# Kernel tuning notes

Measured on AMD Instinct MI355X. Metric: run time of the kernel, lower is better.

## Reference

```python
import jax, jax.numpy as jnp
import numpy as np

MAX_NEIGHBORS = 10
D = 1024
N = 16384

def setup_inputs() -> dict:
    key = jax.random.key(0)
    ks = jax.random.split(key, 12)
    s = 0.05
    inp = {
        'target_embedding': jax.random.normal(ks[0], (D,), jnp.float32),
        'all_embeddings': jax.random.normal(ks[1], (N, D), jnp.float32),
        'similarity_matrix': jax.random.normal(ks[2], (N, N), jnp.float32),
        # attention_net: Linear(2D->D), ReLU, Linear(D->1)
        'W_att1': jax.random.normal(ks[3], (2 * D, D), jnp.float32) * s,
        'b_att1': jnp.zeros((D,), jnp.float32),
        'W_att2': jax.random.normal(ks[4], (D, 1), jnp.float32) * s,
        'b_att2': jnp.zeros((1,), jnp.float32),
        # neighbor_count_net: Linear(D->D//2), ReLU, Linear(D//2->1), Sigmoid
        'W_cnt1': jax.random.normal(ks[5], (D, D // 2), jnp.float32) * s,
        'b_cnt1': jnp.zeros((D // 2,), jnp.float32),
        'W_cnt2': jax.random.normal(ks[6], (D // 2, 1), jnp.float32) * s,
        'b_cnt2': jnp.zeros((1,), jnp.float32),
        'target_idx': 123,
    }
    return inp

def reference(target_embedding, all_embeddings, similarity_matrix,
              W_att1, b_att1, W_att2, b_att2,
              W_cnt1, b_cnt1, W_cnt2, b_cnt2, target_idx):
    # dynamic neighbor count: int(sigmoid(mlp(x)) * max_neighbors), clamped to [1, max_neighbors]
    h = jax.nn.relu(target_embedding @ W_cnt1 + b_cnt1)
    frac = jax.nn.sigmoid(h @ W_cnt2 + b_cnt2)[0]
    dynamic_k = jnp.clip(jnp.floor(frac * MAX_NEIGHBORS).astype(jnp.int32), 1, MAX_NEIGHBORS)

    # top-(K+1) over the target's similarity row; statically sized, mask to dynamic_k
    row = similarity_matrix[target_idx]
    _, top_idx = jax.lax.top_k(row, MAX_NEIGHBORS + 1)  # [K+1]
    # stable compaction: move target_idx (if present) to the end, keep order otherwise
    order = jnp.where(top_idx == target_idx, MAX_NEIGHBORS + 1, jnp.arange(MAX_NEIGHBORS + 1))
    neighbor_idx = top_idx[jnp.argsort(order)][:MAX_NEIGHBORS]  # [K]
    valid = jnp.arange(MAX_NEIGHBORS) < dynamic_k              # [K]

    neighbor_emb = all_embeddings[neighbor_idx]                 # [K, D]
    target_exp = jnp.broadcast_to(target_embedding, (MAX_NEIGHBORS, D))
    pair = jnp.concatenate([target_exp, neighbor_emb], axis=-1)  # [K, 2D]
    scores = (jax.nn.relu(pair @ W_att1 + b_att1) @ W_att2 + b_att2)[:, 0]  # [K]
    scores = jnp.where(valid, scores, -jnp.inf)
    weights = jax.nn.softmax(scores)                            # zeros at invalid slots
    aggregated = weights @ neighbor_emb                         # [D]
    return aggregated, weights, neighbor_idx, weights
```

## Files before the change

kernel.cpp:

```cpp
#include <hip/hip_runtime.h>
#include <math.h>

#define NN 16384
#define DD 1024
#define HD 512

#define WS_DK  0
#define WS_NB  4
#define WS_SC  16
#define WS_UP  64
#define WS_HP  (64 + 32 * 1024)

__global__ void __launch_bounds__(512) k1(const float* __restrict__ x,
                                          const float* __restrict__ W1,
                                          const float* __restrict__ Wc1,
                                          const float* __restrict__ sim,
                                          const int* __restrict__ tidx,
                                          float* __restrict__ ws,
                                          float* __restrict__ out) {
    const int t = threadIdx.x;
    const int b = blockIdx.x;
    const int lane = t & 63, wave = t >> 6;

    if (b > 0 && b <= 64) {
        __shared__ float xs[32];
        const int idx = b - 1, ic = idx >> 1, jc = idx & 1;
        const int ibase = ic * 32;
        if (t < 32) xs[t] = x[ibase + t];
        __syncthreads();
        const int j = jc * 512 + t;
        float acc = 0.f;
        const float* W = W1 + (size_t)ibase * DD + j;
        #pragma unroll 8
        for (int ii = 0; ii < 32; ++ii) acc += xs[ii] * W[(size_t)ii * DD];
        ws[WS_UP + ic * DD + j] = acc;
        return;
    }
    if (b > 64) {
        __shared__ float xs[32];
        const int c = b - 65;
        const int ibase = c * 32;
        if (t < 32) xs[t] = x[ibase + t];
        __syncthreads();
        float acc = 0.f;
        const float* W = Wc1 + (size_t)ibase * HD + t;
        #pragma unroll 8
        for (int ii = 0; ii < 32; ++ii) acc += xs[ii] * W[(size_t)ii * HD];
        ws[WS_HP + c * HD + t] = acc;
        return;
    }

    if (t < 10) ws[WS_SC + t] = 0.f;

    const int tgt = tidx[0];
    const float4* row4 = (const float4*)(sim + (size_t)tgt * NN);
    float vals[32];
    #pragma unroll
    for (int c = 0; c < 8; ++c) {
        float4 v = row4[c * 512 + t];
        vals[c * 4 + 0] = v.x; vals[c * 4 + 1] = v.y;
        vals[c * 4 + 2] = v.z; vals[c * 4 + 3] = v.w;
    }
    unsigned used = 0u;
    float bv = -INFINITY; int bs = 0;
    #pragma unroll
    for (int s = 0; s < 32; ++s) if (vals[s] > bv) { bv = vals[s]; bs = s; }

    __shared__ float wlv[8][11];
    __shared__ int   wli[8][11];

    for (int it = 0; it < 11; ++it) {
        float cv = bv;
        int   cg = (bs >> 2) * 2048 + t * 4 + (bs & 3);
        #pragma unroll
        for (int off = 32; off > 0; off >>= 1) {
            float ov = __shfl_down(cv, off);
            int   og = __shfl_down(cg, off);
            if (ov > cv || (ov == cv && og < cg)) { cv = ov; cg = og; }
        }
        const int wg = __shfl(cg, 0);
        if (lane == 0) { wlv[wave][it] = cv; wli[wave][it] = cg; }
        if (((wg >> 2) & 511) == t) {
            used |= 1u << (((wg >> 11) << 2) | (wg & 3));
            bv = -INFINITY; bs = 0;
            #pragma unroll
            for (int s = 0; s < 32; ++s) {
                float v = ((used >> s) & 1u) ? -INFINITY : vals[s];
                if (v > bv) { bv = v; bs = s; }
            }
        }
    }
    __syncthreads();
    if (t == 0) {
        int head[8] = {0, 0, 0, 0, 0, 0, 0, 0};
        int toplist[11];
        for (int it = 0; it < 11; ++it) {
            float fv = -INFINITY; int fg = 0x7fffffff; int fw = 0;
            #pragma unroll
            for (int w = 0; w < 8; ++w) {
                float v = wlv[w][head[w]];
                int   g = wli[w][head[w]];
                if (v > fv || (v == fv && g < fg)) { fv = v; fg = g; fw = w; }
            }
            toplist[it] = fg;
            head[fw] = head[fw] < 10 ? head[fw] + 1 : 10;
        }
        int cnt = 0;
        int* nbp = (int*)ws + WS_NB;
        for (int i = 0; i < 11 && cnt < 10; ++i) {
            int v = toplist[i];
            if (v != tgt) { nbp[cnt] = v; out[1034 + cnt] = (float)v; ++cnt; }
        }
    }
}

__global__ void __launch_bounds__(512) k2(const float* __restrict__ emb,
                                          const float* __restrict__ W1,
                                          const float* __restrict__ ba1,
                                          const float* __restrict__ W2,
                                          const float* __restrict__ bc1,
                                          const float* __restrict__ Wc2,
                                          const float* __restrict__ bc2,
                                          float* __restrict__ ws) {
    const int t = threadIdx.x;
    const int b = blockIdx.x;
    const int lane = t & 63, wave = t >> 6;

    __shared__ int    nb[10];
    __shared__ float4 es4[10][256];
    __shared__ float  red[32][16][11];
    __shared__ float  ured[32][17];
    __shared__ float  scr[16][10];
    __shared__ float  redp[8];

    if (b == 64) {
        float s = 0.f;
        #pragma unroll 8
        for (int c = 0; c < 32; ++c) s += ws[WS_HP + c * HD + t];
        float v = fmaxf(s + bc1[t], 0.f) * Wc2[t];
        #pragma unroll
        for (int off = 32; off > 0; off >>= 1) v += __shfl_down(v, off);
        if (lane == 0) redp[wave] = v;
        __syncthreads();
        if (t == 0) {
            float z = bc2[0];
            #pragma unroll
            for (int w = 0; w < 8; ++w) z += redp[w];
            float frac = 1.f / (1.f + expf(-z));
            int dk = (int)floorf(frac * 10.f);
            ((int*)ws)[WS_DK] = dk < 1 ? 1 : (dk > 10 ? 10 : dk);
        }
        return;
    }

    const int jl  = t & 15;
    const int seg = t >> 4;
    const int jg  = b * 16 + jl;

    if (t < 10) nb[t] = ((const int*)ws)[WS_NB + t];
    __syncthreads();
    #pragma unroll
    for (int i = t; i < 2560; i += 512) {
        int k = i >> 8, c = i & 255;
        es4[k][c] = ((const float4*)(emb + (size_t)nb[k] * DD))[c];
    }
    ured[seg][jl] = ws[WS_UP + seg * DD + jg];
    __syncthreads();

    float acc[10];
    #pragma unroll
    for (int k = 0; k < 10; ++k) acc[k] = 0.f;
    const float* Wb = W1 + (size_t)(1024 + seg * 32) * DD + jg;
    for (int c = 0; c < 8; ++c) {
        float4 ev[10];
        #pragma unroll
        for (int k = 0; k < 10; ++k) ev[k] = es4[k][seg * 8 + c];
        #pragma unroll
        for (int q = 0; q < 4; ++q) {
            const float wb = Wb[(size_t)(c * 4 + q) * DD];
            #pragma unroll
            for (int k = 0; k < 10; ++k)
                acc[k] += reinterpret_cast<const float*>(&ev[k])[q] * wb;
        }
    }
    #pragma unroll
    for (int k = 0; k < 10; ++k) red[seg][jl][k] = acc[k];
    __syncthreads();

    if (t < 160) {
        const int k = t >> 4, jj = t & 15;
        float s = 0.f;
        #pragma unroll 8
        for (int g = 0; g < 32; ++g) s += red[g][jj][k];
        float u = 0.f;
        #pragma unroll 8
        for (int g = 0; g < 32; ++g) u += ured[g][jj];
        scr[jj][k] = fmaxf(u + s + ba1[b * 16 + jj], 0.f) * W2[b * 16 + jj];
    }
    __syncthreads();
    if (t < 10) {
        float s = 0.f;
        #pragma unroll
        for (int c = 0; c < 16; ++c) s += scr[c][t];
        atomicAdd(&ws[WS_SC + t], s);
    }
}

__global__ void __launch_bounds__(1024) k3(const float* __restrict__ emb,
                                           const float* __restrict__ ba2,
                                           float* __restrict__ ws,
                                           float* __restrict__ out) {
    const int t = threadIdx.x;
    __shared__ float wl[10];
    __shared__ int   nb[10];
    if (t < 10) nb[t] = ((const int*)ws)[WS_NB + t];
    if (t == 0) {
        const int dk = ((const int*)ws)[WS_DK];
        float sv[10];
        float m = -INFINITY;
        for (int k = 0; k < 10; ++k) {
            float s = ws[WS_SC + k] + ba2[0];
            sv[k] = (k < dk) ? s : -INFINITY;
            if (sv[k] > m) m = sv[k];
        }
        float sum = 0.f;
        for (int k = 0; k < 10; ++k) { sv[k] = expf(sv[k] - m); sum += sv[k]; }
        for (int k = 0; k < 10; ++k) wl[k] = sv[k] / sum;
    }
    __syncthreads();
    float a = 0.f;
    #pragma unroll
    for (int k = 0; k < 10; ++k) a += wl[k] * emb[(size_t)nb[k] * DD + t];
    out[t] = a;
    if (t < 10) { out[1024 + t] = wl[t]; out[1044 + t] = wl[t]; }
}

extern "C" void kernel_launch(void* const* d_in, const int* in_sizes, int n_in,
                              void* d_out, int out_size, void* d_ws, size_t ws_size,
                              hipStream_t stream) {
    const float* x    = (const float*)d_in[0];
    const float* emb  = (const float*)d_in[1];
    const float* sim  = (const float*)d_in[2];
    const float* W1   = (const float*)d_in[3];
    const float* ba1  = (const float*)d_in[4];
    const float* W2   = (const float*)d_in[5];
    const float* ba2  = (const float*)d_in[6];
    const float* Wc1  = (const float*)d_in[7];
    const float* bc1  = (const float*)d_in[8];
    const float* Wc2  = (const float*)d_in[9];
    const float* bc2  = (const float*)d_in[10];
    const int*   tidx = (const int*)d_in[11];
    float* out = (float*)d_out;
    float* ws  = (float*)d_ws;

    hipLaunchKernelGGL(k1, dim3(97), dim3(512),  0, stream, x, W1, Wc1, sim, tidx, ws, out);
    hipLaunchKernelGGL(k2, dim3(65), dim3(512),  0, stream, emb, W1, ba1, W2, bc1, Wc2, bc2, ws);
    hipLaunchKernelGGL(k3, dim3(1),  dim3(1024), 0, stream, emb, ba2, ws, out);
}
```

Baseline: 38.42 us.

## Fuse top-k, attention GEMV and count MLP into one kernel, drop a launch

Merges the three-kernel pipeline into two. Each of the 64 attention blocks now recomputes the top-k over the similarity row and the target half of the first attention layer itself. This removes the separate partial-sum pass and the atomics on scores, which now go to per-block partial slots. The count MLP runs in 32 extra blocks that each produce a partial logit, and the final kernel reduces both sets of partials. The cost is redundant top-k work: every block reads the 64 KB similarity row and runs the selection, in exchange for one fewer launch and its sync point.

```diff
diff --git a/kernel.cpp b/kernel.cpp
--- a/kernel.cpp
+++ b/kernel.cpp
@@ -5,16 +5,19 @@
 #define DD 1024
 #define HD 512
 
-#define WS_DK  0
 #define WS_NB  4
-#define WS_SC  16
-#define WS_UP  64
-#define WS_HP  (64 + 32 * 1024)
-
-__global__ void __launch_bounds__(512) k1(const float* __restrict__ x,
+#define WS_ZP  32
+#define WS_SCP 64
+
+__global__ void __launch_bounds__(512) ka(const float* __restrict__ x,
+                                          const float* __restrict__ emb,
+                                          const float* __restrict__ sim,
                                           const float* __restrict__ W1,
+                                          const float* __restrict__ ba1,
+                                          const float* __restrict__ W2,
                                           const float* __restrict__ Wc1,
-                                          const float* __restrict__ sim,
+                                          const float* __restrict__ bc1,
+                                          const float* __restrict__ Wc2,
                                           const int* __restrict__ tidx,
                                           float* __restrict__ ws,
                                           float* __restrict__ out) {
@@ -22,154 +25,121 @@
     const int b = blockIdx.x;
     const int lane = t & 63, wave = t >> 6;
 
-    if (b > 0 && b <= 64) {
-        __shared__ float xs[32];
-        const int idx = b - 1, ic = idx >> 1, jc = idx & 1;
-        const int ibase = ic * 32;
-        if (t < 32) xs[t] = x[ibase + t];
-        __syncthreads();
-        const int j = jc * 512 + t;
-        float acc = 0.f;
-        const float* W = W1 + (size_t)ibase * DD + j;
+    __shared__ float xsl[1024];
+
+    if (b >= 64) {
+        __shared__ float credc[32][17];
+        __shared__ float hs[16];
+        const int c = b - 64;
+        xsl[t] = x[t]; xsl[t + 512] = x[t + 512];
+        __syncthreads();
+        const int jl = t & 15, seg = t >> 4;
+        const int jg = c * 16 + jl;
+        float a = 0.f;
+        const float* Wc = Wc1 + (size_t)(seg * 32) * HD + jg;
         #pragma unroll 8
-        for (int ii = 0; ii < 32; ++ii) acc += xs[ii] * W[(size_t)ii * DD];
-        ws[WS_UP + ic * DD + j] = acc;
+        for (int ii = 0; ii < 32; ++ii) a += xsl[seg * 32 + ii] * Wc[(size_t)ii * HD];
+        credc[seg][jl] = a;
+        __syncthreads();
+        if (t < 16) {
+            float s = 0.f;
+            #pragma unroll 8
+            for (int g = 0; g < 32; ++g) s += credc[g][t];
+            hs[t] = fmaxf(s + bc1[c * 16 + t], 0.f) * Wc2[c * 16 + t];
+        }
+        __syncthreads();
+        if (t == 0) {
+            float z = 0.f;
+            #pragma unroll
+            for (int j = 0; j < 16; ++j) z += hs[j];
+            ws[WS_ZP + c] = z;
+        }
         return;
     }
-    if (b > 64) {
-        __shared__ float xs[32];
-        const int c = b - 65;
-        const int ibase = c * 32;
-        if (t < 32) xs[t] = x[ibase + t];
-        __syncthreads();
-        float acc = 0.f;
-        const float* W = Wc1 + (size_t)ibase * HD + t;
-        #pragma unroll 8
-        for (int ii = 0; ii < 32; ++ii) acc += xs[ii] * W[(size_t)ii * HD];
-        ws[WS_HP + c * HD + t] = acc;
-        return;
-    }
-
-    if (t < 10) ws[WS_SC + t] = 0.f;
-
-    const int tgt = tidx[0];
-    const float4* row4 = (const float4*)(sim + (size_t)tgt * NN);
-    float vals[32];
-    #pragma unroll
-    for (int c = 0; c < 8; ++c) {
-        float4 v = row4[c * 512 + t];
-        vals[c * 4 + 0] = v.x; vals[c * 4 + 1] = v.y;
-        vals[c * 4 + 2] = v.z; vals[c * 4 + 3] = v.w;
-    }
-    unsigned used = 0u;
-    float bv = -INFINITY; int bs = 0;
-    #pragma unroll
-    for (int s = 0; s < 32; ++s) if (vals[s] > bv) { bv = vals[s]; bs = s; }
-
-    __shared__ float wlv[8][11];
-    __shared__ int   wli[8][11];
-
-    for (int it = 0; it < 11; ++it) {
-        float cv = bv;
-        int   cg = (bs >> 2) * 2048 + t * 4 + (bs & 3);
-        #pragma unroll
-        for (int off = 32; off > 0; off >>= 1) {
-            float ov = __shfl_down(cv, off);
-            int   og = __shfl_down(cg, off);
-            if (ov > cv || (ov == cv && og < cg)) { cv = ov; cg = og; }
-        }
-        const int wg = __shfl(cg, 0);
-        if (lane == 0) { wlv[wave][it] = cv; wli[wave][it] = cg; }
-        if (((wg >> 2) & 511) == t) {
-            used |= 1u << (((wg >> 11) << 2) | (wg & 3));
-            bv = -INFINITY; bs = 0;
-            #pragma unroll
-            for (int s = 0; s < 32; ++s) {
-                float v = ((used >> s) & 1u) ? -INFINITY : vals[s];
-                if (v > bv) { bv = v; bs = s; }
-            }
-        }
-    }
-    __syncthreads();
-    if (t == 0) {
-        int head[8] = {0, 0, 0, 0, 0, 0, 0, 0};
-        int toplist[11];
-        for (int it = 0; it < 11; ++it) {
-            float fv = -INFINITY; int fg = 0x7fffffff; int fw = 0;
-            #pragma unroll
-            for (int w = 0; w < 8; ++w) {
-                float v = wlv[w][head[w]];
-                int   g = wli[w][head[w]];
-                if (v > fv || (v == fv && g < fg)) { fv = v; fg = g; fw = w; }
-            }
-            toplist[it] = fg;
-            head[fw] = head[fw] < 10 ? head[fw] + 1 : 10;
-        }
-        int cnt = 0;
-        int* nbp = (int*)ws + WS_NB;
-        for (int i = 0; i < 11 && cnt < 10; ++i) {
-            int v = toplist[i];
-            if (v != tgt) { nbp[cnt] = v; out[1034 + cnt] = (float)v; ++cnt; }
-        }
-    }
-}
-
-__global__ void __launch_bounds__(512) k2(const float* __restrict__ emb,
-                                          const float* __restrict__ W1,
-                                          const float* __restrict__ ba1,
-                                          const float* __restrict__ W2,
-                                          const float* __restrict__ bc1,
-                                          const float* __restrict__ Wc2,
-                                          const float* __restrict__ bc2,
-                                          float* __restrict__ ws) {
-    const int t = threadIdx.x;
-    const int b = blockIdx.x;
-    const int lane = t & 63, wave = t >> 6;
-
-    __shared__ int    nb[10];
+
+    __shared__ float  wlv[8][11];
+    __shared__ int    wli[8][11];
+    __shared__ int    nbsh[10];
     __shared__ float4 es4[10][256];
     __shared__ float  red[32][16][11];
-    __shared__ float  ured[32][17];
     __shared__ float  scr[16][10];
-    __shared__ float  redp[8];
-
-    if (b == 64) {
-        float s = 0.f;
-        #pragma unroll 8
-        for (int c = 0; c < 32; ++c) s += ws[WS_HP + c * HD + t];
-        float v = fmaxf(s + bc1[t], 0.f) * Wc2[t];
-        #pragma unroll
-        for (int off = 32; off > 0; off >>= 1) v += __shfl_down(v, off);
-        if (lane == 0) redp[wave] = v;
+
+    const int tgt = tidx[0];
+    {
+        const float4* row4 = (const float4*)(sim + (size_t)tgt * NN);
+        float vals[32];
+        #pragma unroll
+        for (int c = 0; c < 8; ++c) {
+            float4 v = row4[c * 512 + t];
+            vals[c*4+0] = v.x; vals[c*4+1] = v.y; vals[c*4+2] = v.z; vals[c*4+3] = v.w;
+        }
+        unsigned used = 0u;
+        float bv = -INFINITY; int bs = 0;
+        #pragma unroll
+        for (int s = 0; s < 32; ++s) if (vals[s] > bv) { bv = vals[s]; bs = s; }
+
+        for (int it = 0; it < 11; ++it) {
+            float cv = bv;
+            int   cg2 = (bs >> 2) * 2048 + t * 4 + (bs & 3);
+            #pragma unroll
+            for (int off = 32; off > 0; off >>= 1) {
+                float ov = __shfl_down(cv, off);
+                int   og = __shfl_down(cg2, off);
+                if (ov > cv || (ov == cv && og < cg2)) { cv = ov; cg2 = og; }
+            }
+            const int wg = __shfl(cg2, 0);
+            if (lane == 0) { wlv[wave][it] = cv; wli[wave][it] = cg2; }
+            if (((wg >> 2) & 511) == t) {
+                used |= 1u << (((wg >> 11) << 2) | (wg & 3));
+                bv = -INFINITY; bs = 0;
+                #pragma unroll
+                for (int s = 0; s < 32; ++s) {
+                    float v = ((used >> s) & 1u) ? -INFINITY : vals[s];
+                    if (v > bv) { bv = v; bs = s; }
+                }
+            }
+        }
         __syncthreads();
         if (t == 0) {
-            float z = bc2[0];
-            #pragma unroll
-            for (int w = 0; w < 8; ++w) z += redp[w];
-            float frac = 1.f / (1.f + expf(-z));
-            int dk = (int)floorf(frac * 10.f);
-            ((int*)ws)[WS_DK] = dk < 1 ? 1 : (dk > 10 ? 10 : dk);
-        }
-        return;
-    }
-
-    const int jl  = t & 15;
-    const int seg = t >> 4;
-    const int jg  = b * 16 + jl;
-
-    if (t < 10) nb[t] = ((const int*)ws)[WS_NB + t];
+            int head[8] = {0,0,0,0,0,0,0,0};
+            int toplist[11];
+            for (int it = 0; it < 11; ++it) {
+                float fv = -INFINITY; int fg = 0x7fffffff; int fw = 0;
+                #pragma unroll
+                for (int w = 0; w < 8; ++w) {
+                    float v = wlv[w][head[w]];
+                    int   g = wli[w][head[w]];
+                    if (v > fv || (v == fv && g < fg)) { fv = v; fg = g; fw = w; }
+                }
+                toplist[it] = fg;
+                head[fw] = head[fw] < 10 ? head[fw] + 1 : 10;
+            }
+            int cnt = 0;
+            for (int i = 0; i < 11 && cnt < 10; ++i) {
+                int v = toplist[i];
+                if (v != tgt) {
+                    nbsh[cnt] = v;
+                    if (b == 0) { ((int*)ws)[WS_NB + cnt] = v; out[1034 + cnt] = (float)v; }
+                    ++cnt;
+                }
+            }
+        }
+    }
+    xsl[t] = x[t]; xsl[t + 512] = x[t + 512];
     __syncthreads();
     #pragma unroll
     for (int i = t; i < 2560; i += 512) {
         int k = i >> 8, c = i & 255;
-        es4[k][c] = ((const float4*)(emb + (size_t)nb[k] * DD))[c];
-    }
-    ured[seg][jl] = ws[WS_UP + seg * DD + jg];
-    __syncthreads();
-
-    float acc[10];
-    #pragma unroll
-    for (int k = 0; k < 10; ++k) acc[k] = 0.f;
+        es4[k][c] = ((const float4*)(emb + (size_t)nbsh[k] * DD))[c];
+    }
+    __syncthreads();
+
+    const int jl = t & 15, seg = t >> 4;
+    const int jg = b * 16 + jl;
+    float acc[11];
+    #pragma unroll
+    for (int k = 0; k < 11; ++k) acc[k] = 0.f;
+    const float* Wt = W1 + (size_t)(seg * 32) * DD + jg;
     const float* Wb = W1 + (size_t)(1024 + seg * 32) * DD + jg;
     for (int c = 0; c < 8; ++c) {
         float4 ev[10];
@@ -177,24 +147,24 @@
         for (int k = 0; k < 10; ++k) ev[k] = es4[k][seg * 8 + c];
         #pragma unroll
         for (int q = 0; q < 4; ++q) {
-            const float wb = Wb[(size_t)(c * 4 + q) * DD];
+            const int row = c * 4 + q;
+            const float wt = Wt[(size_t)row * DD];
+            const float wb = Wb[(size_t)row * DD];
+            acc[10] += xsl[seg * 32 + row] * wt;
             #pragma unroll
             for (int k = 0; k < 10; ++k)
                 acc[k] += reinterpret_cast<const float*>(&ev[k])[q] * wb;
         }
     }
     #pragma unroll
-    for (int k = 0; k < 10; ++k) red[seg][jl][k] = acc[k];
+    for (int k = 0; k < 11; ++k) red[seg][jl][k] = acc[k];
     __syncthreads();
 
     if (t < 160) {
         const int k = t >> 4, jj = t & 15;
-        float s = 0.f;
+        float s = 0.f, u = 0.f;
         #pragma unroll 8
-        for (int g = 0; g < 32; ++g) s += red[g][jj][k];
-        float u = 0.f;
-        #pragma unroll 8
-        for (int g = 0; g < 32; ++g) u += ured[g][jj];
+        for (int g = 0; g < 32; ++g) { s += red[g][jj][k]; u += red[g][jj][10]; }
         scr[jj][k] = fmaxf(u + s + ba1[b * 16 + jj], 0.f) * W2[b * 16 + jj];
     }
     __syncthreads();
@@ -202,24 +172,39 @@
         float s = 0.f;
         #pragma unroll
         for (int c = 0; c < 16; ++c) s += scr[c][t];
-        atomicAdd(&ws[WS_SC + t], s);
+        ws[WS_SCP + b * 10 + t] = s;
     }
 }
 
-__global__ void __launch_bounds__(1024) k3(const float* __restrict__ emb,
+__global__ void __launch_bounds__(1024) kb(const float* __restrict__ emb,
                                            const float* __restrict__ ba2,
+                                           const float* __restrict__ bc2,
                                            float* __restrict__ ws,
                                            float* __restrict__ out) {
     const int t = threadIdx.x;
+    __shared__ float sred[10][65];
+    __shared__ float zps[32];
     __shared__ float wl[10];
     __shared__ int   nb[10];
     if (t < 10) nb[t] = ((const int*)ws)[WS_NB + t];
+    if (t < 32) zps[t] = ws[WS_ZP + t];
+    if (t < 640) { const int k = t >> 6, g = t & 63; sred[k][g] = ws[WS_SCP + g * 10 + k]; }
+    __syncthreads();
+    for (int off = 32; off > 0; off >>= 1) {
+        if (t < 640) { const int k = t >> 6, g = t & 63; if (g < off) sred[k][g] += sred[k][g + off]; }
+        __syncthreads();
+    }
     if (t == 0) {
-        const int dk = ((const int*)ws)[WS_DK];
+        float z = bc2[0];
+        #pragma unroll
+        for (int c = 0; c < 32; ++c) z += zps[c];
+        const float frac = 1.f / (1.f + expf(-z));
+        int dk = (int)floorf(frac * 10.f);
+        dk = dk < 1 ? 1 : (dk > 10 ? 10 : dk);
         float sv[10];
         float m = -INFINITY;
         for (int k = 0; k < 10; ++k) {
-            float s = ws[WS_SC + k] + ba2[0];
+            float s = sred[k][0] + ba2[0];
             sv[k] = (k < dk) ? s : -INFINITY;
             if (sv[k] > m) m = sv[k];
         }
@@ -253,7 +238,7 @@
     float* out = (float*)d_out;
     float* ws  = (float*)d_ws;
 
-    hipLaunchKernelGGL(k1, dim3(97), dim3(512),  0, stream, x, W1, Wc1, sim, tidx, ws, out);
-    hipLaunchKernelGGL(k2, dim3(65), dim3(512),  0, stream, emb, W1, ba1, W2, bc1, Wc2, bc2, ws);
-    hipLaunchKernelGGL(k3, dim3(1),  dim3(1024), 0, stream, emb, ba2, ws, out);
+    hipLaunchKernelGGL(ka, dim3(96), dim3(512),  0, stream,
+                       x, emb, sim, W1, ba1, W2, Wc1, bc1, Wc2, tidx, ws, out);
+    hipLaunchKernelGGL(kb, dim3(1),  dim3(1024), 0, stream, emb, ba2, bc2, ws, out);
 }
```

After: 38.00 us. About the same (-1.1%).
